# Kernel optimization log

Hardware: AMD Instinct MI355X
Metric: run time of the kernel (lower is better)

The kernel has to match this reference:

```python
import jax, jax.numpy as jnp
import numpy as np

DIM = 1024
HEADS = 16
HEAD_DIM = DIM // HEADS
B, N = 2, 2048


def setup_inputs() -> dict:
    key = jax.random.key(0)
    k1, k2, k3, k4 = jax.random.split(key, 4)
    x = jax.random.normal(k1, (B, N, DIM), dtype=jnp.float32)
    # torch Linear weights: shape (out_features, in_features), y = x @ W.T + b
    w_qkv = jax.random.normal(k2, (3 * DIM, DIM), dtype=jnp.float32) * (DIM ** -0.5)
    w_proj = jax.random.normal(k3, (DIM, DIM), dtype=jnp.float32) * (DIM ** -0.5)
    b_proj = jax.random.normal(k4, (DIM,), dtype=jnp.float32) * 0.01
    return {"x": x, "w_qkv": w_qkv, "w_proj": w_proj, "b_proj": b_proj}


def reference(x, w_qkv, w_proj, b_proj):
    Bb, Nn, D = x.shape
    scale = HEAD_DIM ** -0.5
    qkv = x @ w_qkv.T                                # [B, N, 3D]
    qkv = qkv.reshape(Bb, Nn, 3, HEADS, HEAD_DIM)
    qkv = jnp.transpose(qkv, (2, 0, 3, 1, 4))        # [3, B, H, N, hd]
    q, k, v = qkv[0], qkv[1], qkv[2]
    attn = jnp.einsum('bhqd,bhkd->bhqk', q, k) * scale
    attn = jax.nn.softmax(attn, axis=-1)
    out = jnp.einsum('bhqk,bhkd->bhqd', attn, v)     # [B, H, N, hd]
    out = jnp.transpose(out, (0, 2, 1, 3)).reshape(Bb, Nn, D)
    return out @ w_proj.T + b_proj
```

## Files before the change

### kernel.cpp

```cpp
#include <hip/hip_runtime.h>
#include <hip/hip_bf16.h>
#include <cstdint>
#include <cstddef>

using u16 = unsigned short;
using u32 = uint32_t;
using f32x4  = __attribute__((ext_vector_type(4))) float;
using bf16x8 = __attribute__((ext_vector_type(8))) __bf16;
using s16x4  = __attribute__((ext_vector_type(4))) short;

#define D_MODEL 1024
#define N_HEADS 16
#define HD      64
#define SEQ     2048
#define QKV_LD  3072
#define K2SCALE 0.18033688011112042f

__device__ __forceinline__ u16 f2b(float f) {
  union { float f; u32 u; } v; v.f = f;
  u32 r = 0x7FFFu + ((v.u >> 16) & 1u);
  return (u16)((v.u + r) >> 16);
}

__device__ __forceinline__ u32 pkbf16(float a, float b) {
  union { __hip_bfloat162 h; u32 u; } c;
  c.h = __float22bfloat162_rn(float2{a, b});
  return c.u;
}

#define MFMA16(A, B, C) __builtin_amdgcn_mfma_f32_16x16x16bf16_1k(A, B, C, 0, 0, 0)

__device__ __forceinline__ void gld16(const u16* g, u16* l) {
  __builtin_amdgcn_global_load_lds(
      (const __attribute__((address_space(1))) void*)g,
      (__attribute__((address_space(3))) void*)l, 16, 0, 0);
}

__global__ void cast3_bf16(const float* __restrict__ x, const float* __restrict__ wq,
                           const float* __restrict__ wp, u16* __restrict__ dst) {
  int i = blockIdx.x * blockDim.x + threadIdx.x;
  const float* src;
  int off;
  if (blockIdx.x < 4096)      { src = x;  off = 0; }
  else if (blockIdx.x < 7168) { src = wq; off = 4096 * 256; }
  else                        { src = wp; off = 7168 * 256; }
  float4 f = ((const float4*)src)[i - off];
  u32 lo = pkbf16(f.x, f.y), hi = pkbf16(f.z, f.w);
  uint2 o = {lo, hi};
  ((uint2*)dst)[i] = o;
}

template<int OUTMODE, int MT>
__launch_bounds__(256, 3)
__global__ void gemm_nt(const u16* __restrict__ A, const u16* __restrict__ B,
                        u16* __restrict__ Ob, float* __restrict__ Of,
                        const float* __restrict__ bias, int N, int K) {
  __shared__ __attribute__((aligned(16))) u16 sA[2][MT * 32];
  __shared__ __attribute__((aligned(16))) u16 sB[2][128 * 32];

  const int tid  = threadIdx.x;
  const int lane = tid & 63;
  const int w    = tid >> 6;
  const int qd   = lane >> 4;
  const int ln   = lane & 15;
  constexpr int MI = MT / 32;
  const int wm   = (w >> 1) * (MT / 2);
  const int wn   = (w & 1) * 64;
  const int m0   = blockIdx.y * MT;
  const int n0   = blockIdx.x * 128;

  auto stage = [&](int kk, int buf) {
    int k0 = kk * 32;
    #pragma unroll
    for (int c = 0; c < MT / 64; ++c) {
      int sbase = w * MT + c * 64;
      int s = sbase + lane;
      int row = s >> 2, col = (s & 3) * 8;
      gld16(A + (size_t)(m0 + row) * K + k0 + col, &sA[buf][sbase * 8]);
    }
    #pragma unroll
    for (int c = 0; c < 2; ++c) {
      int sbase = w * 128 + c * 64;
      int s = sbase + lane;
      int row = s >> 2, col = (s & 3) * 8;
      gld16(B + (size_t)(n0 + row) * K + k0 + col, &sB[buf][sbase * 8]);
    }
  };

  f32x4 acc[MI][4] = {};
  const int NK = K >> 5;
  stage(0, 0);

  for (int kk = 0; kk < NK; ++kk) {
    const int cur = kk & 1;
    __syncthreads();
    if (kk + 1 < NK) stage(kk + 1, cur ^ 1);

    bf16x8 af[MI], bfm[4];
    #pragma unroll
    for (int i = 0; i < MI; ++i)
      af[i] = *(const bf16x8*)&sA[cur][(wm + i * 16 + ln) * 32 + qd * 8];
    #pragma unroll
    for (int j = 0; j < 4; ++j)
      bfm[j] = *(const bf16x8*)&sB[cur][(wn + j * 16 + ln) * 32 + qd * 8];
    #pragma unroll
    for (int i = 0; i < MI; ++i)
      #pragma unroll
      for (int j = 0; j < 4; ++j)
        acc[i][j] = __builtin_amdgcn_mfma_f32_16x16x32_bf16(af[i], bfm[j], acc[i][j], 0, 0, 0);
  }

  #pragma unroll
  for (int i = 0; i < MI; ++i) {
    #pragma unroll
    for (int j = 0; j < 4; ++j) {
      #pragma unroll
      for (int r = 0; r < 4; ++r) {
        int row = m0 + wm + i * 16 + qd * 4 + r;
        int col = n0 + wn + j * 16 + ln;
        float v = acc[i][j][r];
        if (OUTMODE == 0) {
          if (col < D_MODEL) v *= K2SCALE;
          Ob[(size_t)row * N + col] = f2b(v);
        } else {
          Of[(size_t)row * N + col] = v + bias[col];
        }
      }
    }
  }
}

__launch_bounds__(256, 3)
__global__ void attn_kernel(const u16* __restrict__ qkv, u16* __restrict__ outb) {
  __shared__ __attribute__((aligned(16))) u16 smem[16384];
  u16 (*sK)[2][64 * 32] = (u16(*)[2][64 * 32])smem;
  u32 (*sVT)[64 * 32]   = (u32(*)[64 * 32])(smem + 8192);

  const int tid  = threadIdx.x;
  const int lane = tid & 63;
  const int w    = tid >> 6;
  const int qd   = lane >> 4;
  const int ln   = lane & 15;
  const int qp   = blockIdx.x;
  const int h    = blockIdx.y & 15;
  const int b    = blockIdx.y >> 4;
  const size_t tokbase = (size_t)b * SEQ;
  const int q0   = qp * 128;
  const int qoff = h * HD;
  const int koff = D_MODEL + h * HD;
  const int voff = 2 * D_MODEL + h * HD;

  bf16x8 aq[2][2];
  #pragma unroll
  for (int c2 = 0; c2 < 2; ++c2)
    #pragma unroll
    for (int hf = 0; hf < 2; ++hf)
      aq[c2][hf] = *(const bf16x8*)(qkv + (tokbase + q0 + c2 * 64 + w * 16 + ln) * QKV_LD
                                    + qoff + hf * 32 + qd * 8);

  auto stageK = [&](int kt, int buf) {
    #pragma unroll
    for (int hf = 0; hf < 2; ++hf) {
      int s = w * 64 + lane;
      int row = s >> 2, col = (s & 3) * 8;
      gld16(qkv + (tokbase + kt * 64 + row) * QKV_LD + koff + hf * 32 + col,
            &sK[buf][hf][w * 512]);
    }
  };
  auto loadV = [&](int kt, uint4& va, uint4& vb) {
    int tp = tid & 31, d0 = (tid >> 5) * 8;
    const u16* g0 = qkv + (tokbase + kt * 64 + tp * 2) * QKV_LD + voff + d0;
    va = *(const uint4*)g0;
    vb = *(const uint4*)(g0 + QKV_LD);
  };
  auto writeV = [&](int buf, const uint4& va, const uint4& vb) {
    int tp = tid & 31, d0 = (tid >> 5) * 8;
    const u32* a  = (const u32*)&va;
    const u32* bb = (const u32*)&vb;
    #pragma unroll
    for (int e = 0; e < 4; ++e) {
      sVT[buf][(d0 + 2 * e    ) * 32 + (tp ^ (e << 3)    )] =
          __builtin_amdgcn_perm(bb[e], a[e], 0x05040100u);
      sVT[buf][(d0 + 2 * e + 1) * 32 + (tp ^ (e << 3) ^ 4)] =
          __builtin_amdgcn_perm(bb[e], a[e], 0x07060302u);
    }
  };

  stageK(0, 0);
  uint4 va, vb;
  loadV(0, va, vb);
  writeV(0, va, vb);
  loadV(1, va, vb);

  f32x4 accOT[2][4] = {};
  float psum[2] = {0.f, 0.f};
  const int tsw = (ln & 7) << 2;

  for (int kt = 0; kt < 32; ++kt) {
    const int cur = kt & 1, nxt = cur ^ 1;
    __syncthreads();
    if (kt < 31) { stageK(kt + 1, nxt); writeV(nxt, va, vb); }
    if (kt < 30) { loadV(kt + 2, va, vb); }

    #pragma unroll
    for (int cb = 0; cb < 4; ++cb) {
      bf16x8 ak0 = *(const bf16x8*)&sK[cur][0][(cb * 16 + ln) * 32 + qd * 8];
      bf16x8 ak1 = *(const bf16x8*)&sK[cur][1][(cb * 16 + ln) * 32 + qd * 8];
      f32x4 st[2];
      #pragma unroll
      for (int c2 = 0; c2 < 2; ++c2) {
        f32x4 z = {0.f, 0.f, 0.f, 0.f};
        f32x4 t = __builtin_amdgcn_mfma_f32_16x16x32_bf16(ak0, aq[c2][0], z, 0, 0, 0);
        st[c2]  = __builtin_amdgcn_mfma_f32_16x16x32_bf16(ak1, aq[c2][1], t, 0, 0, 0);
      }
      s16x4 pf[2];
      #pragma unroll
      for (int c2 = 0; c2 < 2; ++c2) {
        float p0 = __builtin_amdgcn_exp2f(st[c2][0]);
        float p1 = __builtin_amdgcn_exp2f(st[c2][1]);
        float p2 = __builtin_amdgcn_exp2f(st[c2][2]);
        float p3 = __builtin_amdgcn_exp2f(st[c2][3]);
        psum[c2] += (p0 + p1) + (p2 + p3);
        union { u32 d[2]; s16x4 v; } pk;
        pk.d[0] = pkbf16(p0, p1);
        pk.d[1] = pkbf16(p2, p3);
        pf[c2] = pk.v;
      }
      #pragma unroll
      for (int ob = 0; ob < 4; ++ob) {
        s16x4 vf = *(const s16x4*)&sVT[cur][(ob * 16 + ln) * 32
                                           + ((cb * 8 + qd * 2) ^ tsw)];
        accOT[0][ob] = MFMA16(vf, pf[0], accOT[0][ob]);
        accOT[1][ob] = MFMA16(vf, pf[1], accOT[1][ob]);
      }
    }
  }

  #pragma unroll
  for (int c2 = 0; c2 < 2; ++c2) {
    float s = psum[c2];
    s += __shfl_xor(s, 16, 64);
    s += __shfl_xor(s, 32, 64);
    psum[c2] = 1.0f / s;
  }

  u16* sOut = smem;
  __syncthreads();
  #pragma unroll
  for (int c2 = 0; c2 < 2; ++c2)
    #pragma unroll
    for (int ob = 0; ob < 4; ++ob) {
      u32 lo = pkbf16(accOT[c2][ob][0] * psum[c2], accOT[c2][ob][1] * psum[c2]);
      u32 hi = pkbf16(accOT[c2][ob][2] * psum[c2], accOT[c2][ob][3] * psum[c2]);
      ((u32*)sOut)[(c2 * 64 + w * 16 + ln) * 36 + ob * 8 + qd * 2    ] = lo;
      ((u32*)sOut)[(c2 * 64 + w * 16 + ln) * 36 + ob * 8 + qd * 2 + 1] = hi;
    }
  __syncthreads();
  #pragma unroll
  for (int it = 0; it < 4; ++it) {
    int idx = it * 256 + tid;
    int token = idx >> 3, chunk = idx & 7;
    uint4 v = *(const uint4*)&sOut[token * 72 + chunk * 8];
    *(uint4*)&outb[(tokbase + q0 + token) * D_MODEL + h * HD + chunk * 8] = v;
  }
}

extern "C" void kernel_launch(void* const* d_in, const int* in_sizes, int n_in,
                              void* d_out, int out_size, void* d_ws, size_t ws_size,
                              hipStream_t stream) {
  const float* x      = (const float*)d_in[0];
  const float* w_qkv  = (const float*)d_in[1];
  const float* w_proj = (const float*)d_in[2];
  const float* b_proj = (const float*)d_in[3];
  float* out = (float*)d_out;

  u16* ws     = (u16*)d_ws;
  u16* xb     = ws;
  u16* wqkvb  = xb    + (size_t)4096 * 1024;
  u16* wprojb = wqkvb + (size_t)3072 * 1024;
  u16* qkvb   = wprojb + (size_t)1024 * 1024;
  u16* attnb  = qkvb  + (size_t)4096 * 3072;

  cast3_bf16<<<8192, 256, 0, stream>>>(x, w_qkv, w_proj, xb);

  gemm_nt<0, 128><<<dim3(24, 32), 256, 0, stream>>>(xb, wqkvb, qkvb, nullptr, nullptr, 3072, 1024);

  attn_kernel<<<dim3(16, 32), 256, 0, stream>>>(qkvb, attnb);

  gemm_nt<1, 64><<<dim3(8, 64), 256, 0, stream>>>(attnb, wprojb, nullptr, out, b_proj, 1024, 1024);
}
```

Before: 186.1 us.

## Write V transposed and swizzled from QKV GEMM epilogue, stage via async LDS loads

After: 193.0 us. 3.7% more time.

```diff
diff --git a/kernel.cpp b/kernel.cpp
--- a/kernel.cpp
+++ b/kernel.cpp
@@ -13,7 +13,7 @@
 #define N_HEADS 16
 #define HD      64
 #define SEQ     2048
-#define QKV_LD  3072
+#define QK_LD   2048
 #define K2SCALE 0.18033688011112042f
 
 __device__ __forceinline__ u16 f2b(float f) {
@@ -53,8 +53,9 @@
 template<int OUTMODE, int MT>
 __launch_bounds__(256, 3)
 __global__ void gemm_nt(const u16* __restrict__ A, const u16* __restrict__ B,
-                        u16* __restrict__ Ob, float* __restrict__ Of,
-                        const float* __restrict__ bias, int N, int K) {
+                        u16* __restrict__ ObQK, u16* __restrict__ ObVT,
+                        float* __restrict__ Of, const float* __restrict__ bias,
+                        int N, int K) {
   __shared__ __attribute__((aligned(16))) u16 sA[2][MT * 32];
   __shared__ __attribute__((aligned(16))) u16 sB[2][128 * 32];
 
@@ -120,8 +121,16 @@
         int col = n0 + wn + j * 16 + ln;
         float v = acc[i][j][r];
         if (OUTMODE == 0) {
-          if (col < D_MODEL) v *= K2SCALE;
-          Ob[(size_t)row * N + col] = f2b(v);
+          if (n0 < 2048) {
+            if (col < D_MODEL) v *= K2SCALE;
+            ObQK[(size_t)row * QK_LD + col] = f2b(v);
+          } else {
+            int dcol = col - 2048;
+            int dd   = dcol & 63;
+            size_t idx = (size_t)dcol * 4096 + (row & ~63)
+                       + 2 * (((row >> 1) & 31) ^ ((dd & 7) << 2)) + (row & 1);
+            ObVT[idx] = f2b(v);
+          }
         } else {
           Of[(size_t)row * N + col] = v + bias[col];
         }
@@ -131,7 +140,8 @@
 }
 
 __launch_bounds__(256, 3)
-__global__ void attn_kernel(const u16* __restrict__ qkv, u16* __restrict__ outb) {
+__global__ void attn_kernel(const u16* __restrict__ qk, const u16* __restrict__ vT,
+                            u16* __restrict__ outb) {
   __shared__ __attribute__((aligned(16))) u16 smem[16384];
   u16 (*sK)[2][64 * 32] = (u16(*)[2][64 * 32])smem;
   u32 (*sVT)[64 * 32]   = (u32(*)[64 * 32])(smem + 8192);
@@ -148,14 +158,13 @@
   const int q0   = qp * 128;
   const int qoff = h * HD;
   const int koff = D_MODEL + h * HD;
-  const int voff = 2 * D_MODEL + h * HD;
 
   bf16x8 aq[2][2];
   #pragma unroll
   for (int c2 = 0; c2 < 2; ++c2)
     #pragma unroll
     for (int hf = 0; hf < 2; ++hf)
-      aq[c2][hf] = *(const bf16x8*)(qkv + (tokbase + q0 + c2 * 64 + w * 16 + ln) * QKV_LD
+      aq[c2][hf] = *(const bf16x8*)(qk + (tokbase + q0 + c2 * 64 + w * 16 + ln) * QK_LD
                                     + qoff + hf * 32 + qd * 8);
 
   auto stageK = [&](int kt, int buf) {
@@ -163,34 +172,21 @@
     for (int hf = 0; hf < 2; ++hf) {
       int s = w * 64 + lane;
       int row = s >> 2, col = (s & 3) * 8;
-      gld16(qkv + (tokbase + kt * 64 + row) * QKV_LD + koff + hf * 32 + col,
+      gld16(qk + (tokbase + kt * 64 + row) * QK_LD + koff + hf * 32 + col,
             &sK[buf][hf][w * 512]);
     }
   };
-  auto loadV = [&](int kt, uint4& va, uint4& vb) {
-    int tp = tid & 31, d0 = (tid >> 5) * 8;
-    const u16* g0 = qkv + (tokbase + kt * 64 + tp * 2) * QKV_LD + voff + d0;
-    va = *(const uint4*)g0;
-    vb = *(const uint4*)(g0 + QKV_LD);
+  auto stageV = [&](int kt, int buf) {
+    #pragma unroll
+    for (int c = 0; c < 2; ++c) {
+      int d = w * 8 + c * 32 + (lane >> 3);
+      gld16(vT + (size_t)(h * 64 + d) * 4096 + (b * SEQ + kt * 64) + (lane & 7) * 8,
+            (u16*)(sVT[buf] + (w * 8 + c * 32) * 32));
+    }
   };
-  auto writeV = [&](int buf, const uint4& va, const uint4& vb) {
-    int tp = tid & 31, d0 = (tid >> 5) * 8;
-    const u32* a  = (const u32*)&va;
-    const u32* bb = (const u32*)&vb;
-    #pragma unroll
-    for (int e = 0; e < 4; ++e) {
-      sVT[buf][(d0 + 2 * e    ) * 32 + (tp ^ (e << 3)    )] =
-          __builtin_amdgcn_perm(bb[e], a[e], 0x05040100u);
-      sVT[buf][(d0 + 2 * e + 1) * 32 + (tp ^ (e << 3) ^ 4)] =
-          __builtin_amdgcn_perm(bb[e], a[e], 0x07060302u);
-    }
-  };
 
   stageK(0, 0);
-  uint4 va, vb;
-  loadV(0, va, vb);
-  writeV(0, va, vb);
-  loadV(1, va, vb);
+  stageV(0, 0);
 
   f32x4 accOT[2][4] = {};
   float psum[2] = {0.f, 0.f};
@@ -199,8 +195,7 @@
   for (int kt = 0; kt < 32; ++kt) {
     const int cur = kt & 1, nxt = cur ^ 1;
     __syncthreads();
-    if (kt < 31) { stageK(kt + 1, nxt); writeV(nxt, va, vb); }
-    if (kt < 30) { loadV(kt + 2, va, vb); }
+    if (kt < 31) { stageK(kt + 1, nxt); stageV(kt + 1, nxt); }
 
     #pragma unroll
     for (int cb = 0; cb < 4; ++cb) {
@@ -278,14 +273,17 @@
   u16* xb     = ws;
   u16* wqkvb  = xb    + (size_t)4096 * 1024;
   u16* wprojb = wqkvb + (size_t)3072 * 1024;
-  u16* qkvb   = wprojb + (size_t)1024 * 1024;
-  u16* attnb  = qkvb  + (size_t)4096 * 3072;
+  u16* qkb    = wprojb + (size_t)1024 * 1024;
+  u16* vTb    = qkb   + (size_t)4096 * 2048;
+  u16* attnb  = vTb   + (size_t)1024 * 4096;
 
   cast3_bf16<<<8192, 256, 0, stream>>>(x, w_qkv, w_proj, xb);
 
-  gemm_nt<0, 128><<<dim3(24, 32), 256, 0, stream>>>(xb, wqkvb, qkvb, nullptr, nullptr, 3072, 1024);
-
-  attn_kernel<<<dim3(16, 32), 256, 0, stream>>>(qkvb, attnb);
-
-  gemm_nt<1, 64><<<dim3(8, 64), 256, 0, stream>>>(attnb, wprojb, nullptr, out, b_proj, 1024, 1024);
-}
+  gemm_nt<0, 128><<<dim3(24, 32), 256, 0, stream>>>(
+      xb, wqkvb, qkb, vTb, nullptr, nullptr, 3072, 1024);
+
+  attn_kernel<<<dim3(16, 32), 256, 0, stream>>>(qkb, vTb, attnb);
+
+  gemm_nt<1, 64><<<dim3(8, 64), 256, 0, stream>>>(
+      attnb, wprojb, nullptr, nullptr, out, b_proj, 1024, 1024);
+}
```

## Split attention key range across two warp groups with LDS reduction

Applied to the files above, without the earlier changes.

After: 199.6 us. +7.3%, slower.

```diff
diff --git a/kernel.cpp b/kernel.cpp
--- a/kernel.cpp
+++ b/kernel.cpp
@@ -130,15 +130,16 @@
   }
 }
 
-__launch_bounds__(256, 3)
+__launch_bounds__(512, 4)
 __global__ void attn_kernel(const u16* __restrict__ qkv, u16* __restrict__ outb) {
-  __shared__ __attribute__((aligned(16))) u16 smem[16384];
-  u16 (*sK)[2][64 * 32] = (u16(*)[2][64 * 32])smem;
-  u32 (*sVT)[64 * 32]   = (u32(*)[64 * 32])(smem + 8192);
+  __shared__ __attribute__((aligned(16))) u16 smem[32768];
 
   const int tid  = threadIdx.x;
   const int lane = tid & 63;
   const int w    = tid >> 6;
+  const int wl   = w & 3;
+  const int h2   = w >> 2;
+  const int t256 = tid & 255;
   const int qd   = lane >> 4;
   const int ln   = lane & 15;
   const int qp   = blockIdx.x;
@@ -150,38 +151,41 @@
   const int koff = D_MODEL + h * HD;
   const int voff = 2 * D_MODEL + h * HD;
 
+  u16* sK  = smem + h2 * 16384;
+  u32* sVT = (u32*)(smem + h2 * 16384 + 8192);
+
   bf16x8 aq[2][2];
   #pragma unroll
   for (int c2 = 0; c2 < 2; ++c2)
     #pragma unroll
     for (int hf = 0; hf < 2; ++hf)
-      aq[c2][hf] = *(const bf16x8*)(qkv + (tokbase + q0 + c2 * 64 + w * 16 + ln) * QKV_LD
+      aq[c2][hf] = *(const bf16x8*)(qkv + (tokbase + q0 + c2 * 64 + wl * 16 + ln) * QKV_LD
                                     + qoff + hf * 32 + qd * 8);
 
   auto stageK = [&](int kt, int buf) {
     #pragma unroll
     for (int hf = 0; hf < 2; ++hf) {
-      int s = w * 64 + lane;
+      int s = wl * 64 + lane;
       int row = s >> 2, col = (s & 3) * 8;
-      gld16(qkv + (tokbase + kt * 64 + row) * QKV_LD + koff + hf * 32 + col,
-            &sK[buf][hf][w * 512]);
+      gld16(qkv + (tokbase + (h2 * 16 + kt) * 64 + row) * QKV_LD + koff + hf * 32 + col,
+            &sK[buf * 4096 + hf * 2048 + wl * 512]);
     }
   };
   auto loadV = [&](int kt, uint4& va, uint4& vb) {
-    int tp = tid & 31, d0 = (tid >> 5) * 8;
-    const u16* g0 = qkv + (tokbase + kt * 64 + tp * 2) * QKV_LD + voff + d0;
+    int tp = t256 & 31, d0 = (t256 >> 5) * 8;
+    const u16* g0 = qkv + (tokbase + (h2 * 16 + kt) * 64 + tp * 2) * QKV_LD + voff + d0;
     va = *(const uint4*)g0;
     vb = *(const uint4*)(g0 + QKV_LD);
   };
   auto writeV = [&](int buf, const uint4& va, const uint4& vb) {
-    int tp = tid & 31, d0 = (tid >> 5) * 8;
+    int tp = t256 & 31, d0 = (t256 >> 5) * 8;
     const u32* a  = (const u32*)&va;
     const u32* bb = (const u32*)&vb;
     #pragma unroll
     for (int e = 0; e < 4; ++e) {
-      sVT[buf][(d0 + 2 * e    ) * 32 + (tp ^ (e << 3)    )] =
+      sVT[buf * 2048 + (d0 + 2 * e    ) * 32 + (tp ^ (e << 3)    )] =
           __builtin_amdgcn_perm(bb[e], a[e], 0x05040100u);
-      sVT[buf][(d0 + 2 * e + 1) * 32 + (tp ^ (e << 3) ^ 4)] =
+      sVT[buf * 2048 + (d0 + 2 * e + 1) * 32 + (tp ^ (e << 3) ^ 4)] =
           __builtin_amdgcn_perm(bb[e], a[e], 0x07060302u);
     }
   };
@@ -196,16 +200,16 @@
   float psum[2] = {0.f, 0.f};
   const int tsw = (ln & 7) << 2;
 
-  for (int kt = 0; kt < 32; ++kt) {
+  for (int kt = 0; kt < 16; ++kt) {
     const int cur = kt & 1, nxt = cur ^ 1;
     __syncthreads();
-    if (kt < 31) { stageK(kt + 1, nxt); writeV(nxt, va, vb); }
-    if (kt < 30) { loadV(kt + 2, va, vb); }
+    if (kt < 15) { stageK(kt + 1, nxt); writeV(nxt, va, vb); }
+    if (kt < 14) { loadV(kt + 2, va, vb); }
 
     #pragma unroll
     for (int cb = 0; cb < 4; ++cb) {
-      bf16x8 ak0 = *(const bf16x8*)&sK[cur][0][(cb * 16 + ln) * 32 + qd * 8];
-      bf16x8 ak1 = *(const bf16x8*)&sK[cur][1][(cb * 16 + ln) * 32 + qd * 8];
+      bf16x8 ak0 = *(const bf16x8*)&sK[cur * 4096 +        (cb * 16 + ln) * 32 + qd * 8];
+      bf16x8 ak1 = *(const bf16x8*)&sK[cur * 4096 + 2048 + (cb * 16 + ln) * 32 + qd * 8];
       f32x4 st[2];
       #pragma unroll
       for (int c2 = 0; c2 < 2; ++c2) {
@@ -228,8 +232,8 @@
       }
       #pragma unroll
       for (int ob = 0; ob < 4; ++ob) {
-        s16x4 vf = *(const s16x4*)&sVT[cur][(ob * 16 + ln) * 32
-                                           + ((cb * 8 + qd * 2) ^ tsw)];
+        s16x4 vf = *(const s16x4*)&sVT[cur * 2048 + (ob * 16 + ln) * 32
+                                       + ((cb * 8 + qd * 2) ^ tsw)];
         accOT[0][ob] = MFMA16(vf, pf[0], accOT[0][ob]);
         accOT[1][ob] = MFMA16(vf, pf[1], accOT[1][ob]);
       }
@@ -241,27 +245,56 @@
     float s = psum[c2];
     s += __shfl_xor(s, 16, 64);
     s += __shfl_xor(s, 32, 64);
-    psum[c2] = 1.0f / s;
-  }
-
-  u16* sOut = smem;
+    psum[c2] = s;
+  }
+
+  float* pex = (float*)smem;
+  float* ps  = (float*)(smem + 16384);
+  u16*  sOut = smem + 18432;
+
   __syncthreads();
-  #pragma unroll
-  for (int c2 = 0; c2 < 2; ++c2)
-    #pragma unroll
-    for (int ob = 0; ob < 4; ++ob) {
-      u32 lo = pkbf16(accOT[c2][ob][0] * psum[c2], accOT[c2][ob][1] * psum[c2]);
-      u32 hi = pkbf16(accOT[c2][ob][2] * psum[c2], accOT[c2][ob][3] * psum[c2]);
-      ((u32*)sOut)[(c2 * 64 + w * 16 + ln) * 36 + ob * 8 + qd * 2    ] = lo;
-      ((u32*)sOut)[(c2 * 64 + w * 16 + ln) * 36 + ob * 8 + qd * 2 + 1] = hi;
-    }
+  if (w >= 4) {
+    #pragma unroll
+    for (int c2 = 0; c2 < 2; ++c2) {
+      #pragma unroll
+      for (int ob = 0; ob < 4; ++ob)
+        *(f32x4*)&pex[(wl * 2 + c2) * 1024 + (ob * 64 + qd * 16 + ln) * 4] =
+            accOT[c2][ob];
+      if (qd == 0) ps[(wl * 2 + c2) * 16 + ln] = psum[c2];
+    }
+  }
   __syncthreads();
-  #pragma unroll
-  for (int it = 0; it < 4; ++it) {
-    int idx = it * 256 + tid;
-    int token = idx >> 3, chunk = idx & 7;
-    uint4 v = *(const uint4*)&sOut[token * 72 + chunk * 8];
-    *(uint4*)&outb[(tokbase + q0 + token) * D_MODEL + h * HD + chunk * 8] = v;
+  if (w < 4) {
+    float rinv[2];
+    #pragma unroll
+    for (int c2 = 0; c2 < 2; ++c2) {
+      #pragma unroll
+      for (int ob = 0; ob < 4; ++ob) {
+        f32x4 part = *(const f32x4*)&pex[(wl * 2 + c2) * 1024
+                                         + (ob * 64 + qd * 16 + ln) * 4];
+        accOT[c2][ob] += part;
+      }
+      rinv[c2] = 1.0f / (psum[c2] + ps[(wl * 2 + c2) * 16 + ln]);
+    }
+    #pragma unroll
+    for (int c2 = 0; c2 < 2; ++c2)
+      #pragma unroll
+      for (int ob = 0; ob < 4; ++ob) {
+        u32 lo = pkbf16(accOT[c2][ob][0] * rinv[c2], accOT[c2][ob][1] * rinv[c2]);
+        u32 hi = pkbf16(accOT[c2][ob][2] * rinv[c2], accOT[c2][ob][3] * rinv[c2]);
+        ((u32*)sOut)[(c2 * 64 + wl * 16 + ln) * 36 + ob * 8 + qd * 2    ] = lo;
+        ((u32*)sOut)[(c2 * 64 + wl * 16 + ln) * 36 + ob * 8 + qd * 2 + 1] = hi;
+      }
+  }
+  __syncthreads();
+  if (w < 4) {
+    #pragma unroll
+    for (int it = 0; it < 4; ++it) {
+      int idx = it * 256 + tid;
+      int token = idx >> 3, chunk = idx & 7;
+      uint4 v = *(const uint4*)&sOut[token * 72 + chunk * 8];
+      *(uint4*)&outb[(tokbase + q0 + token) * D_MODEL + h * HD + chunk * 8] = v;
+    }
   }
 }
 
@@ -285,7 +318,7 @@
 
   gemm_nt<0, 128><<<dim3(24, 32), 256, 0, stream>>>(xb, wqkvb, qkvb, nullptr, nullptr, 3072, 1024);
 
-  attn_kernel<<<dim3(16, 32), 256, 0, stream>>>(qkvb, attnb);
+  attn_kernel<<<dim3(16, 32), 512, 0, stream>>>(qkvb, attnb);
 
   gemm_nt<1, 64><<<dim3(8, 64), 256, 0, stream>>>(attnb, wprojb, nullptr, out, b_proj, 1024, 1024);
 }
```
